# Kernel optimization log

Measured on AMD Instinct MI355X. Metric: run time of the kernel, lower is better.

Reference implementation:

```python
import jax, jax.numpy as jnp
import numpy as np

B, N, M = 4096, 512, 64
SEQ_W = 8
HID, CTRL_OUT = 256, 128
SHIFT_VEC = (-1, 0, 1)
L = len(SHIFT_VEC)
PARAM_SIZE = M + 1 + 1 + L + 1  # k(M), beta, g, s(L), gamma
# circular-shift gather indices: idx[i, j] = (i + shift_vec[j]) mod N
IDX = np.mod(np.arange(N)[:, None] + np.array(SHIFT_VEC)[None, :], N)


def setup_inputs() -> dict:
    key = jax.random.key(0)
    ks = jax.random.split(key, 12)
    def w(k, shape, fan_in):
        return jax.random.normal(k, shape, jnp.float32) / np.sqrt(fan_in).astype(np.float32)
    in_size = SEQ_W + 1 + M  # controller input: x (seq_width+1) + prev_read (M)
    wr = jax.random.uniform(ks[3], (B, N), jnp.float32)
    wr = wr / wr.sum(axis=1, keepdims=True)
    ww = jax.random.uniform(ks[4], (B, N), jnp.float32)
    ww = ww / ww.sum(axis=1, keepdims=True)
    return {
        "x": jax.random.normal(ks[0], (B, SEQ_W + 1), jnp.float32),
        "prev_read": jax.random.normal(ks[1], (B, M), jnp.float32),
        "bank": jax.random.uniform(ks[2], (B, N, M), jnp.float32) * 0.1 + 1e-6,
        "w_read": wr,
        "w_write": ww,
        "ctrl_W0": w(ks[5], (in_size, HID), in_size), "ctrl_b0": jnp.zeros(HID, jnp.float32),
        "ctrl_W1": w(ks[6], (HID, HID), HID), "ctrl_b1": jnp.zeros(HID, jnp.float32),
        "ctrl_Wout": w(ks[7], (HID, CTRL_OUT), HID), "ctrl_bout": jnp.zeros(CTRL_OUT, jnp.float32),
        "repr_W": w(ks[8], (CTRL_OUT, 2 * PARAM_SIZE + 2 * M), CTRL_OUT),
        "repr_b": jnp.zeros(2 * PARAM_SIZE + 2 * M, jnp.float32),
        "out_W": w(ks[9], (CTRL_OUT + M, SEQ_W), CTRL_OUT + M),
        "out_b": jnp.zeros(SEQ_W, jnp.float32),
    }


def _split(v):
    # k [B,M], beta [B,1], g [B,1], s [B,L], gamma [B,1]
    return v[:, :M], v[:, M:M + 1], v[:, M + 1:M + 2], v[:, M + 2:M + 2 + L], v[:, -1:]


def _address(param, w_prev, bank):
    k, beta, g, s, gamma = param
    kt = jnp.tanh(k)
    # cosine similarity along M (torch CosineSimilarity, eps=1e-8)
    dot = jnp.einsum('bnm,bm->bn', bank, kt)
    denom = jnp.linalg.norm(bank, axis=2) * jnp.linalg.norm(kt, axis=1, keepdims=True)
    cos = dot / jnp.maximum(denom, 1e-8)
    wc = jax.nn.softmax(jax.nn.softplus(beta) * cos, axis=1)
    gg = jax.nn.sigmoid(g)
    wg = gg * wc + (1.0 - gg) * w_prev
    sm = jax.nn.softmax(s, axis=1)
    # vectorized circular shift: ws[b,i] = sum_j wg[b,(i+shift_j)%N] * sm[b,j]
    ws = jnp.einsum('bnl,bl->bn', wg[:, IDX], sm)
    gamma = jax.nn.softplus(gamma) + 1.0
    wsh = ws ** gamma
    return wsh / wsh.sum(axis=1, keepdims=True)


def reference(x, prev_read, bank, w_read, w_write,
              ctrl_W0, ctrl_b0, ctrl_W1, ctrl_b1, ctrl_Wout, ctrl_bout,
              repr_W, repr_b, out_W, out_b):
    ctrl_in = jnp.concatenate([x, prev_read], axis=1)
    h = jax.nn.leaky_relu(ctrl_in @ ctrl_W0 + ctrl_b0)
    h = jax.nn.leaky_relu(h @ ctrl_W1 + ctrl_b1)
    ctrl_out = jnp.tanh(h @ ctrl_Wout + ctrl_bout)
    reprx = ctrl_out @ repr_W + repr_b
    read_param = _split(reprx[:, :PARAM_SIZE])
    write_param = _split(reprx[:, PARAM_SIZE:2 * PARAM_SIZE])
    e = jax.nn.sigmoid(reprx[:, 2 * PARAM_SIZE:2 * PARAM_SIZE + M])
    a = jnp.tanh(reprx[:, 2 * PARAM_SIZE + M:])
    rw = _address(read_param, w_read, bank)
    read = jnp.einsum('bn,bnm->bm', rw, bank)  # memory read
    wwt = _address(write_param, w_write, bank)
    # erase then add: bank - w*e + w*a
    new_bank = bank + wwt[:, :, None] * (a - e)[:, None, :]
    seq_out = jax.nn.sigmoid(jnp.concatenate([ctrl_out, read], axis=1) @ out_W + out_b)
    return seq_out, new_bank
```

## Files before the change

### kernel.cpp

```cpp
#include <hip/hip_runtime.h>
#include <hip/hip_bf16.h>
#include <math.h>

#define B_TOT 4096
#define NN 512
#define MM 64
#define HID 256
#define COUT 128
#define PSZ 70
#define REPRN 268
#define IN_SZ 73
#define WS_STRIDE 352
#define BT 8


__device__ __forceinline__ float sigmoidf_(float v){ return 1.f/(1.f+expf(-v)); }
__device__ __forceinline__ float softplusf_(float v){ return v > 20.f ? v : log1pf(expf(v)); }
__device__ __forceinline__ float leakyf_(float v){ return v >= 0.f ? v : 0.01f*v; }

__device__ __forceinline__ float wave_sum(float v){
  #pragma unroll
  for (int o = 32; o; o >>= 1) v += __shfl_xor(v, o);
  return v;
}
__device__ __forceinline__ float wave_max(float v){
  #pragma unroll
  for (int o = 32; o; o >>= 1) v = fmaxf(v, __shfl_xor(v, o));
  return v;
}

__device__ float block_sum8(float v, float* red){
  v = wave_sum(v);
  int w = threadIdx.x >> 6, l = threadIdx.x & 63;
  __syncthreads();
  if (l == 0) red[w] = v;
  __syncthreads();
  float s = 0.f;
  #pragma unroll
  for (int i = 0; i < 8; ++i) s += red[i];
  return s;
}
__device__ float block_max8(float v, float* red){
  v = wave_max(v);
  int w = threadIdx.x >> 6, l = threadIdx.x & 63;
  __syncthreads();
  if (l == 0) red[w] = v;
  __syncthreads();
  float m = red[0];
  #pragma unroll
  for (int i = 1; i < 8; ++i) m = fmaxf(m, red[i]);
  return m;
}

__global__ __launch_bounds__(256) void k_ctrl(
    const float* __restrict__ x, const float* __restrict__ prev_read,
    const float* __restrict__ W0, const float* __restrict__ b0,
    const float* __restrict__ W1, const float* __restrict__ b1,
    const float* __restrict__ Wout, const float* __restrict__ bout,
    const float* __restrict__ rW, const float* __restrict__ rb,
    float* __restrict__ pws)
{
  __shared__ float cin[BT][80];
  __shared__ float sA[BT][256];
  __shared__ float sB[BT][256];
  __shared__ float sR[BT][272];
  const int t = threadIdx.x;
  const int bbase = blockIdx.x * BT;

  for (int idx = t; idx < BT * IN_SZ; idx += 256){
    int bb = idx / IN_SZ, i = idx - bb * IN_SZ;
    int b = bbase + bb;
    cin[bb][i] = (i < 9) ? x[b * 9 + i] : prev_read[b * MM + (i - 9)];
  }
  __syncthreads();

  {
    float acc[BT];
    #pragma unroll
    for (int bb = 0; bb < BT; ++bb) acc[bb] = 0.f;
    for (int i = 0; i < IN_SZ; ++i){
      float w = W0[i * 256 + t];
      #pragma unroll
      for (int bb = 0; bb < BT; ++bb) acc[bb] += cin[bb][i] * w;
    }
    float bias = b0[t];
    #pragma unroll
    for (int bb = 0; bb < BT; ++bb) sA[bb][t] = leakyf_(acc[bb] + bias);
  }
  __syncthreads();

  {
    float acc[BT];
    #pragma unroll
    for (int bb = 0; bb < BT; ++bb) acc[bb] = 0.f;
    for (int i = 0; i < 256; ++i){
      float w = W1[i * 256 + t];
      #pragma unroll
      for (int bb = 0; bb < BT; ++bb) acc[bb] += sA[bb][i] * w;
    }
    float bias = b1[t];
    #pragma unroll
    for (int bb = 0; bb < BT; ++bb) sB[bb][t] = leakyf_(acc[bb] + bias);
  }
  __syncthreads();

  if (t < COUT){
    float acc[BT];
    #pragma unroll
    for (int bb = 0; bb < BT; ++bb) acc[bb] = 0.f;
    for (int i = 0; i < 256; ++i){
      float w = Wout[i * COUT + t];
      #pragma unroll
      for (int bb = 0; bb < BT; ++bb) acc[bb] += sB[bb][i] * w;
    }
    float bias = bout[t];
    #pragma unroll
    for (int bb = 0; bb < BT; ++bb){
      float v = tanhf(acc[bb] + bias);
      sA[bb][t] = v;
      pws[(size_t)(bbase + bb) * WS_STRIDE + t] = v;
    }
  }
  __syncthreads();

  {
    float acc1[BT], acc2[BT];
    #pragma unroll
    for (int bb = 0; bb < BT; ++bb){ acc1[bb] = 0.f; acc2[bb] = 0.f; }
    const bool has2 = (t + 256) < REPRN;
    for (int i = 0; i < COUT; ++i){
      float w1 = rW[i * REPRN + t];
      float w2 = has2 ? rW[i * REPRN + t + 256] : 0.f;
      #pragma unroll
      for (int bb = 0; bb < BT; ++bb){
        float c = sA[bb][i];
        acc1[bb] += c * w1;
        acc2[bb] += c * w2;
      }
    }
    float r1 = rb[t];
    float r2 = has2 ? rb[t + 256] : 0.f;
    #pragma unroll
    for (int bb = 0; bb < BT; ++bb){
      sR[bb][t] = acc1[bb] + r1;
      if (has2) sR[bb][t + 256] = acc2[bb] + r2;
    }
  }
  __syncthreads();

  for (int bb = 0; bb < BT; ++bb){
    float* pb = pws + (size_t)(bbase + bb) * WS_STRIDE;
    if (t < 64){
      float kt = tanhf(sR[bb][t]);
      pb[128 + t] = kt;
      float s = wave_sum(kt * kt);
      if (t == 0) pb[320] = sqrtf(s);
    } else if (t < 128){
      int m = t - 64;
      float kt = tanhf(sR[bb][PSZ + m]);
      pb[192 + m] = kt;
      float s = wave_sum(kt * kt);
      if (m == 0) pb[328] = sqrtf(s);
    } else if (t < 192){
      int m = t - 128;
      float e = sigmoidf_(sR[bb][2 * PSZ + m]);
      float a = tanhf(sR[bb][2 * PSZ + MM + m]);
      pb[256 + m] = a - e;
    } else if (t == 192 || t == 193){
      int off = (t == 192) ? 0 : PSZ;
      int po  = (t == 192) ? 320 : 328;
      float beta = sR[bb][off + 64];
      float g    = sR[bb][off + 65];
      float s0 = sR[bb][off + 66], s1 = sR[bb][off + 67], s2 = sR[bb][off + 68];
      float gm = sR[bb][off + 69];
      pb[po + 1] = softplusf_(beta);
      pb[po + 2] = sigmoidf_(g);
      float mx = fmaxf(s0, fmaxf(s1, s2));
      float e0 = expf(s0 - mx), e1 = expf(s1 - mx), e2 = expf(s2 - mx);
      float inv = 1.f / (e0 + e1 + e2);
      pb[po + 3] = e0 * inv; pb[po + 4] = e1 * inv; pb[po + 5] = e2 * inv;
      pb[po + 6] = softplusf_(gm) + 1.f;
    }
  }
}

__device__ void address_head(const float* __restrict__ dot, const float* __restrict__ ssv,
                             float knorm, float beta, float g,
                             float sm0, float sm1, float sm2, float gamma,
                             const float* __restrict__ wprev,
                             float* tmp, float* wfin, float* red)
{
  const int t = threadIdx.x;
  float c = dot[t] / fmaxf(sqrtf(ssv[t]) * knorm, 1e-8f);
  float v = beta * c;
  float vmax = block_max8(v, red);
  float e = expf(v - vmax);
  float S = block_sum8(e, red);
  float wg = g * (e / S) + (1.f - g) * wprev[t];
  tmp[t] = wg;
  __syncthreads();
  float ws = tmp[(t + 511) & 511] * sm0 + wg * sm1 + tmp[(t + 1) & 511] * sm2;
  float p = powf(ws, gamma);
  float S2 = block_sum8(p, red);
  wfin[t] = p / S2;
  __syncthreads();
}

__global__ __launch_bounds__(512, 2) void k_head(
    const float* __restrict__ bank,
    const float* __restrict__ w_read, const float* __restrict__ w_write,
    const float* __restrict__ outW, const float* __restrict__ outb,
    const float* __restrict__ pws,
    float* __restrict__ out)
{
  __shared__ float dotr[512], dotw[512], ssv[512], tmp[512], wfr[512], wfw[512];
  __shared__ float red[8];
  __shared__ float readpart[8][64];
  __shared__ float readv[64];

  const int b = blockIdx.x;
  const int t = threadIdx.x;
  const int lane = t & 63, wave = t >> 6;
  const int mg = lane & 15;
  const int rsub = lane >> 4;

  const float* bankB = bank + (size_t)b * (NN * MM);
  const float* pb = pws + (size_t)b * WS_STRIDE;

  const float4 ktr = *(const float4*)(pb + 128 + mg * 4);
  const float4 ktw = *(const float4*)(pb + 192 + mg * 4);

  float4 bank_r[16];
  #pragma unroll
  for (int it = 0; it < 16; ++it){
    int n = it * 32 + wave * 4 + rsub;
    bank_r[it] = *(const float4*)(bankB + n * MM + mg * 4);
  }

  #pragma unroll
  for (int it = 0; it < 16; ++it){
    float4 p = bank_r[it];
    float dr = p.x * ktr.x + p.y * ktr.y + p.z * ktr.z + p.w * ktr.w;
    float dw = p.x * ktw.x + p.y * ktw.y + p.z * ktw.z + p.w * ktw.w;
    float sq = p.x * p.x + p.y * p.y + p.z * p.z + p.w * p.w;
    #pragma unroll
    for (int msk = 1; msk < 16; msk <<= 1){
      dr += __shfl_xor(dr, msk);
      dw += __shfl_xor(dw, msk);
      sq += __shfl_xor(sq, msk);
    }
    if (mg == 0){
      int n = it * 32 + wave * 4 + rsub;
      dotr[n] = dr; dotw[n] = dw; ssv[n] = sq;
    }
  }
  __syncthreads();

  address_head(dotr, ssv, pb[320], pb[321], pb[322], pb[323], pb[324], pb[325], pb[326],
               w_read + (size_t)b * NN, tmp, wfr, red);
  address_head(dotw, ssv, pb[328], pb[329], pb[330], pb[331], pb[332], pb[333], pb[334],
               w_write + (size_t)b * NN, tmp, wfw, red);

  const float4 ae4 = *(const float4*)(pb + 256 + mg * 4);
  float* outBank = out + (size_t)B_TOT * 8 + (size_t)b * (NN * MM);
  float4 racc = make_float4(0.f, 0.f, 0.f, 0.f);
  #pragma unroll
  for (int it = 0; it < 16; ++it){
    int n = it * 32 + wave * 4 + rsub;
    float4 p = bank_r[it];
    float wr = wfr[n], wwn = wfw[n];
    float4 q;
    q.x = p.x + wwn * ae4.x; q.y = p.y + wwn * ae4.y;
    q.z = p.z + wwn * ae4.z; q.w = p.w + wwn * ae4.w;
    *(float4*)(outBank + n * MM + mg * 4) = q;
    racc.x += wr * p.x; racc.y += wr * p.y; racc.z += wr * p.z; racc.w += wr * p.w;
  }
  racc.x += __shfl_xor(racc.x, 16); racc.x += __shfl_xor(racc.x, 32);
  racc.y += __shfl_xor(racc.y, 16); racc.y += __shfl_xor(racc.y, 32);
  racc.z += __shfl_xor(racc.z, 16); racc.z += __shfl_xor(racc.z, 32);
  racc.w += __shfl_xor(racc.w, 16); racc.w += __shfl_xor(racc.w, 32);
  if (lane < 16){
    readpart[wave][mg * 4 + 0] = racc.x;
    readpart[wave][mg * 4 + 1] = racc.y;
    readpart[wave][mg * 4 + 2] = racc.z;
    readpart[wave][mg * 4 + 3] = racc.w;
  }
  __syncthreads();
  if (t < 64){
    float s = 0.f;
    #pragma unroll
    for (int w = 0; w < 8; ++w) s += readpart[w][t];
    readv[t] = s;
  }
  __syncthreads();

  if (t < 64){
    int j = t >> 3, s = t & 7;
    float acc = 0.f;
    for (int i = s; i < COUT; i += 8) acc += pb[i] * outW[i * 8 + j];
    for (int m = s; m < MM; m += 8)   acc += readv[m] * outW[(COUT + m) * 8 + j];
    acc += __shfl_xor(acc, 1);
    acc += __shfl_xor(acc, 2);
    acc += __shfl_xor(acc, 4);
    if (s == 0) out[(size_t)b * 8 + j] = sigmoidf_(acc + outb[j]);
  }
}

extern "C" void kernel_launch(void* const* d_in, const int* in_sizes, int n_in,
                              void* d_out, int out_size, void* d_ws, size_t ws_size,
                              hipStream_t stream) {
  const float* x         = (const float*)d_in[0];
  const float* prev_read = (const float*)d_in[1];
  const float* bank      = (const float*)d_in[2];
  const float* w_read    = (const float*)d_in[3];
  const float* w_write   = (const float*)d_in[4];
  const float* W0        = (const float*)d_in[5];
  const float* b0        = (const float*)d_in[6];
  const float* W1        = (const float*)d_in[7];
  const float* b1        = (const float*)d_in[8];
  const float* Wout      = (const float*)d_in[9];
  const float* bout      = (const float*)d_in[10];
  const float* rW        = (const float*)d_in[11];
  const float* rb        = (const float*)d_in[12];
  const float* outW      = (const float*)d_in[13];
  const float* outb      = (const float*)d_in[14];
  float* out = (float*)d_out;
  float* pws = (float*)d_ws;

  k_ctrl<<<dim3(B_TOT / BT), dim3(256), 0, stream>>>(
      x, prev_read, W0, b0, W1, b1, Wout, bout, rW, rb, pws);
  k_head<<<dim3(B_TOT), dim3(512), 0, stream>>>(
      bank, w_read, w_write, outW, outb, pws, out);
}
```

Baseline: 1.040 ms.

## Fuse read/write addressing heads and transpose controller activations for vector LDS loads

Merges the read-head and write-head addressing into one pass with paired float2 reductions, which cuts the number of block barriers. The softmax max-reduction is replaced by subtracting the known upper bound beta (cosine is at most 1), so one reduction round disappears. Head parameters and previous weights are hoisted into registers before the bank loads. The controller kernel stores activations transposed as [feature][batch], so each step reads them with two float4 LDS loads instead of eight scalar loads. Risks are some extra register pressure and a possible underflow of exp(beta*(c-1)) when beta is large.

```diff
diff --git a/kernel.cpp b/kernel.cpp
--- a/kernel.cpp
+++ b/kernel.cpp
@@ -12,6 +12,7 @@
 #define IN_SZ 73
 #define WS_STRIDE 352
 #define BT 8
+#define CTS 12
 
 
 __device__ __forceinline__ float sigmoidf_(float v){ return 1.f/(1.f+expf(-v)); }
@@ -22,34 +23,6 @@
   #pragma unroll
   for (int o = 32; o; o >>= 1) v += __shfl_xor(v, o);
   return v;
-}
-__device__ __forceinline__ float wave_max(float v){
-  #pragma unroll
-  for (int o = 32; o; o >>= 1) v = fmaxf(v, __shfl_xor(v, o));
-  return v;
-}
-
-__device__ float block_sum8(float v, float* red){
-  v = wave_sum(v);
-  int w = threadIdx.x >> 6, l = threadIdx.x & 63;
-  __syncthreads();
-  if (l == 0) red[w] = v;
-  __syncthreads();
-  float s = 0.f;
-  #pragma unroll
-  for (int i = 0; i < 8; ++i) s += red[i];
-  return s;
-}
-__device__ float block_max8(float v, float* red){
-  v = wave_max(v);
-  int w = threadIdx.x >> 6, l = threadIdx.x & 63;
-  __syncthreads();
-  if (l == 0) red[w] = v;
-  __syncthreads();
-  float m = red[0];
-  #pragma unroll
-  for (int i = 1; i < 8; ++i) m = fmaxf(m, red[i]);
-  return m;
 }
 
 __global__ __launch_bounds__(256) void k_ctrl(
@@ -60,9 +33,10 @@
     const float* __restrict__ rW, const float* __restrict__ rb,
     float* __restrict__ pws)
 {
-  __shared__ float cin[BT][80];
-  __shared__ float sA[BT][256];
-  __shared__ float sB[BT][256];
+  __shared__ float cinT[80][CTS];
+  __shared__ float hAT[256][CTS];
+  __shared__ float hBT[256][CTS];
+  __shared__ float coT[128][CTS];
   __shared__ float sR[BT][272];
   const int t = threadIdx.x;
   const int bbase = blockIdx.x * BT;
@@ -70,80 +44,100 @@
   for (int idx = t; idx < BT * IN_SZ; idx += 256){
     int bb = idx / IN_SZ, i = idx - bb * IN_SZ;
     int b = bbase + bb;
-    cin[bb][i] = (i < 9) ? x[b * 9 + i] : prev_read[b * MM + (i - 9)];
+    cinT[i][bb] = (i < 9) ? x[b * 9 + i] : prev_read[b * MM + (i - 9)];
   }
   __syncthreads();
 
   {
-    float acc[BT];
-    #pragma unroll
-    for (int bb = 0; bb < BT; ++bb) acc[bb] = 0.f;
+    float4 acA = make_float4(0.f,0.f,0.f,0.f), acB = make_float4(0.f,0.f,0.f,0.f);
     for (int i = 0; i < IN_SZ; ++i){
       float w = W0[i * 256 + t];
-      #pragma unroll
-      for (int bb = 0; bb < BT; ++bb) acc[bb] += cin[bb][i] * w;
+      float4 a0 = *(const float4*)&cinT[i][0];
+      float4 a1 = *(const float4*)&cinT[i][4];
+      acA.x += a0.x * w; acA.y += a0.y * w; acA.z += a0.z * w; acA.w += a0.w * w;
+      acB.x += a1.x * w; acB.y += a1.y * w; acB.z += a1.z * w; acB.w += a1.w * w;
     }
     float bias = b0[t];
-    #pragma unroll
-    for (int bb = 0; bb < BT; ++bb) sA[bb][t] = leakyf_(acc[bb] + bias);
+    acA.x = leakyf_(acA.x + bias); acA.y = leakyf_(acA.y + bias);
+    acA.z = leakyf_(acA.z + bias); acA.w = leakyf_(acA.w + bias);
+    acB.x = leakyf_(acB.x + bias); acB.y = leakyf_(acB.y + bias);
+    acB.z = leakyf_(acB.z + bias); acB.w = leakyf_(acB.w + bias);
+    *(float4*)&hAT[t][0] = acA;
+    *(float4*)&hAT[t][4] = acB;
   }
   __syncthreads();
 
   {
-    float acc[BT];
-    #pragma unroll
-    for (int bb = 0; bb < BT; ++bb) acc[bb] = 0.f;
+    float4 acA = make_float4(0.f,0.f,0.f,0.f), acB = make_float4(0.f,0.f,0.f,0.f);
     for (int i = 0; i < 256; ++i){
       float w = W1[i * 256 + t];
-      #pragma unroll
-      for (int bb = 0; bb < BT; ++bb) acc[bb] += sA[bb][i] * w;
+      float4 a0 = *(const float4*)&hAT[i][0];
+      float4 a1 = *(const float4*)&hAT[i][4];
+      acA.x += a0.x * w; acA.y += a0.y * w; acA.z += a0.z * w; acA.w += a0.w * w;
+      acB.x += a1.x * w; acB.y += a1.y * w; acB.z += a1.z * w; acB.w += a1.w * w;
     }
     float bias = b1[t];
-    #pragma unroll
-    for (int bb = 0; bb < BT; ++bb) sB[bb][t] = leakyf_(acc[bb] + bias);
+    acA.x = leakyf_(acA.x + bias); acA.y = leakyf_(acA.y + bias);
+    acA.z = leakyf_(acA.z + bias); acA.w = leakyf_(acA.w + bias);
+    acB.x = leakyf_(acB.x + bias); acB.y = leakyf_(acB.y + bias);
+    acB.z = leakyf_(acB.z + bias); acB.w = leakyf_(acB.w + bias);
+    *(float4*)&hBT[t][0] = acA;
+    *(float4*)&hBT[t][4] = acB;
   }
   __syncthreads();
 
   if (t < COUT){
-    float acc[BT];
-    #pragma unroll
-    for (int bb = 0; bb < BT; ++bb) acc[bb] = 0.f;
+    float4 acA = make_float4(0.f,0.f,0.f,0.f), acB = make_float4(0.f,0.f,0.f,0.f);
     for (int i = 0; i < 256; ++i){
       float w = Wout[i * COUT + t];
-      #pragma unroll
-      for (int bb = 0; bb < BT; ++bb) acc[bb] += sB[bb][i] * w;
+      float4 a0 = *(const float4*)&hBT[i][0];
+      float4 a1 = *(const float4*)&hBT[i][4];
+      acA.x += a0.x * w; acA.y += a0.y * w; acA.z += a0.z * w; acA.w += a0.w * w;
+      acB.x += a1.x * w; acB.y += a1.y * w; acB.z += a1.z * w; acB.w += a1.w * w;
     }
     float bias = bout[t];
-    #pragma unroll
-    for (int bb = 0; bb < BT; ++bb){
-      float v = tanhf(acc[bb] + bias);
-      sA[bb][t] = v;
-      pws[(size_t)(bbase + bb) * WS_STRIDE + t] = v;
-    }
+    acA.x = tanhf(acA.x + bias); acA.y = tanhf(acA.y + bias);
+    acA.z = tanhf(acA.z + bias); acA.w = tanhf(acA.w + bias);
+    acB.x = tanhf(acB.x + bias); acB.y = tanhf(acB.y + bias);
+    acB.z = tanhf(acB.z + bias); acB.w = tanhf(acB.w + bias);
+    *(float4*)&coT[t][0] = acA;
+    *(float4*)&coT[t][4] = acB;
+    pws[(size_t)(bbase + 0) * WS_STRIDE + t] = acA.x;
+    pws[(size_t)(bbase + 1) * WS_STRIDE + t] = acA.y;
+    pws[(size_t)(bbase + 2) * WS_STRIDE + t] = acA.z;
+    pws[(size_t)(bbase + 3) * WS_STRIDE + t] = acA.w;
+    pws[(size_t)(bbase + 4) * WS_STRIDE + t] = acB.x;
+    pws[(size_t)(bbase + 5) * WS_STRIDE + t] = acB.y;
+    pws[(size_t)(bbase + 6) * WS_STRIDE + t] = acB.z;
+    pws[(size_t)(bbase + 7) * WS_STRIDE + t] = acB.w;
   }
   __syncthreads();
 
   {
-    float acc1[BT], acc2[BT];
-    #pragma unroll
-    for (int bb = 0; bb < BT; ++bb){ acc1[bb] = 0.f; acc2[bb] = 0.f; }
+    float4 a1A = make_float4(0.f,0.f,0.f,0.f), a1B = make_float4(0.f,0.f,0.f,0.f);
+    float4 a2A = make_float4(0.f,0.f,0.f,0.f), a2B = make_float4(0.f,0.f,0.f,0.f);
     const bool has2 = (t + 256) < REPRN;
     for (int i = 0; i < COUT; ++i){
       float w1 = rW[i * REPRN + t];
       float w2 = has2 ? rW[i * REPRN + t + 256] : 0.f;
-      #pragma unroll
-      for (int bb = 0; bb < BT; ++bb){
-        float c = sA[bb][i];
-        acc1[bb] += c * w1;
-        acc2[bb] += c * w2;
-      }
+      float4 c0 = *(const float4*)&coT[i][0];
+      float4 c1 = *(const float4*)&coT[i][4];
+      a1A.x += c0.x * w1; a1A.y += c0.y * w1; a1A.z += c0.z * w1; a1A.w += c0.w * w1;
+      a1B.x += c1.x * w1; a1B.y += c1.y * w1; a1B.z += c1.z * w1; a1B.w += c1.w * w1;
+      a2A.x += c0.x * w2; a2A.y += c0.y * w2; a2A.z += c0.z * w2; a2A.w += c0.w * w2;
+      a2B.x += c1.x * w2; a2B.y += c1.y * w2; a2B.z += c1.z * w2; a2B.w += c1.w * w2;
     }
     float r1 = rb[t];
     float r2 = has2 ? rb[t + 256] : 0.f;
-    #pragma unroll
-    for (int bb = 0; bb < BT; ++bb){
-      sR[bb][t] = acc1[bb] + r1;
-      if (has2) sR[bb][t + 256] = acc2[bb] + r2;
+    sR[0][t] = a1A.x + r1; sR[1][t] = a1A.y + r1;
+    sR[2][t] = a1A.z + r1; sR[3][t] = a1A.w + r1;
+    sR[4][t] = a1B.x + r1; sR[5][t] = a1B.y + r1;
+    sR[6][t] = a1B.z + r1; sR[7][t] = a1B.w + r1;
+    if (has2){
+      sR[0][t+256] = a2A.x + r2; sR[1][t+256] = a2A.y + r2;
+      sR[2][t+256] = a2A.z + r2; sR[3][t+256] = a2A.w + r2;
+      sR[4][t+256] = a2B.x + r2; sR[5][t+256] = a2B.y + r2;
+      sR[6][t+256] = a2B.z + r2; sR[7][t+256] = a2B.w + r2;
     }
   }
   __syncthreads();
@@ -184,28 +178,6 @@
   }
 }
 
-__device__ void address_head(const float* __restrict__ dot, const float* __restrict__ ssv,
-                             float knorm, float beta, float g,
-                             float sm0, float sm1, float sm2, float gamma,
-                             const float* __restrict__ wprev,
-                             float* tmp, float* wfin, float* red)
-{
-  const int t = threadIdx.x;
-  float c = dot[t] / fmaxf(sqrtf(ssv[t]) * knorm, 1e-8f);
-  float v = beta * c;
-  float vmax = block_max8(v, red);
-  float e = expf(v - vmax);
-  float S = block_sum8(e, red);
-  float wg = g * (e / S) + (1.f - g) * wprev[t];
-  tmp[t] = wg;
-  __syncthreads();
-  float ws = tmp[(t + 511) & 511] * sm0 + wg * sm1 + tmp[(t + 1) & 511] * sm2;
-  float p = powf(ws, gamma);
-  float S2 = block_sum8(p, red);
-  wfin[t] = p / S2;
-  __syncthreads();
-}
-
 __global__ __launch_bounds__(512, 2) void k_head(
     const float* __restrict__ bank,
     const float* __restrict__ w_read, const float* __restrict__ w_write,
@@ -213,8 +185,9 @@
     const float* __restrict__ pws,
     float* __restrict__ out)
 {
-  __shared__ float dotr[512], dotw[512], ssv[512], tmp[512], wfr[512], wfw[512];
-  __shared__ float red[8];
+  __shared__ float dotr[512], dotw[512], ssv[512];
+  __shared__ float tmpr[512], tmpw[512], wfr[512], wfw[512];
+  __shared__ float2 red2[8];
   __shared__ float readpart[8][64];
   __shared__ float readv[64];
 
@@ -226,6 +199,13 @@
 
   const float* bankB = bank + (size_t)b * (NN * MM);
   const float* pb = pws + (size_t)b * WS_STRIDE;
+
+  const float wpr = w_read [(size_t)b * NN + t];
+  const float wpw = w_write[(size_t)b * NN + t];
+  const float knr = pb[320], br = pb[321], gr = pb[322];
+  const float smr0 = pb[323], smr1 = pb[324], smr2 = pb[325], gmr = pb[326];
+  const float knw = pb[328], bw = pb[329], gw = pb[330];
+  const float smw0 = pb[331], smw1 = pb[332], smw2 = pb[333], gmw = pb[334];
 
   const float4 ktr = *(const float4*)(pb + 128 + mg * 4);
   const float4 ktw = *(const float4*)(pb + 192 + mg * 4);
@@ -256,10 +236,40 @@
   }
   __syncthreads();
 
-  address_head(dotr, ssv, pb[320], pb[321], pb[322], pb[323], pb[324], pb[325], pb[326],
-               w_read + (size_t)b * NN, tmp, wfr, red);
-  address_head(dotw, ssv, pb[328], pb[329], pb[330], pb[331], pb[332], pb[333], pb[334],
-               w_write + (size_t)b * NN, tmp, wfw, red);
+  {
+    float rn = sqrtf(ssv[t]);
+    float cr = dotr[t] / fmaxf(rn * knr, 1e-8f);
+    float cw = dotw[t] / fmaxf(rn * knw, 1e-8f);
+    float er = expf(br * (cr - 1.f));
+    float ew = expf(bw * (cw - 1.f));
+    float sr = er, sw = ew;
+    #pragma unroll
+    for (int o = 32; o; o >>= 1){ sr += __shfl_xor(sr, o); sw += __shfl_xor(sw, o); }
+    if (lane == 0) red2[wave] = make_float2(sr, sw);
+    __syncthreads();
+    float Sr = 0.f, Sw = 0.f;
+    #pragma unroll
+    for (int i = 0; i < 8; ++i){ Sr += red2[i].x; Sw += red2[i].y; }
+    float wgr = gr * (er / Sr) + (1.f - gr) * wpr;
+    float wgw = gw * (ew / Sw) + (1.f - gw) * wpw;
+    tmpr[t] = wgr; tmpw[t] = wgw;
+    __syncthreads();
+    float wsr = tmpr[(t + 511) & 511] * smr0 + wgr * smr1 + tmpr[(t + 1) & 511] * smr2;
+    float wsw = tmpw[(t + 511) & 511] * smw0 + wgw * smw1 + tmpw[(t + 1) & 511] * smw2;
+    float prh = powf(wsr, gmr);
+    float pwh = powf(wsw, gmw);
+    float s2r = prh, s2w = pwh;
+    #pragma unroll
+    for (int o = 32; o; o >>= 1){ s2r += __shfl_xor(s2r, o); s2w += __shfl_xor(s2w, o); }
+    if (lane == 0) red2[wave] = make_float2(s2r, s2w);
+    __syncthreads();
+    float S2r = 0.f, S2w = 0.f;
+    #pragma unroll
+    for (int i = 0; i < 8; ++i){ S2r += red2[i].x; S2w += red2[i].y; }
+    wfr[t] = prh / S2r;
+    wfw[t] = pwh / S2w;
+    __syncthreads();
+  }
 
   const float4 ae4 = *(const float4*)(pb + 256 + mg * 4);
   float* outBank = out + (size_t)B_TOT * 8 + (size_t)b * (NN * MM);
```

Measured after the change: 973.1 us. 1.07x faster.
